# Optimization experiments

Measured on AMD Instinct MI355X. Metric: run time of the kernel, lower is better.

## Reference

```python
import jax, jax.numpy as jnp
import numpy as np

VOCAB = 256
HDC_DIM = 4096
DECAY = 0.95
B, T = 8, 2048


def setup_inputs() -> dict:
    key = jax.random.key(0)
    k_cb, k_idx = jax.random.split(key)
    # bipolar codebook: sign of gaussian, zeros mapped to +1 (prob-0 event but faithful)
    cb = jnp.sign(jax.random.normal(k_cb, (VOCAB, HDC_DIM), dtype=jnp.float32))
    cb = jnp.where(cb == 0, 1.0, cb)
    idx = jax.random.randint(k_idx, (B, T), 0, VOCAB)
    return {"char_codebook": cb, "idx": idx}


def _encode_trigrams(char_codebook, idx):
    chars = char_codebook[idx]                       # (B, T, D)
    chars_m1 = jnp.roll(chars, 1, axis=1).at[:, 0, :].set(0.0)
    chars_m2 = jnp.roll(chars, 2, axis=1).at[:, :2, :].set(0.0)
    trigrams = chars * jnp.roll(chars_m1, 1, axis=-1) * jnp.roll(chars_m2, 2, axis=-1)
    return 0.7 * trigrams + 0.3 * chars


def _decay_matrix(T, dtype):
    i = jnp.arange(T)
    diffs = (i[:, None] - i[None, :]).astype(dtype)  # (T, T)
    m = jnp.where(diffs >= 0, jnp.asarray(DECAY, dtype) ** diffs, 0.0)
    return m / jnp.sum(m, axis=-1, keepdims=True)    # row-normalized causal decay


def reference(char_codebook, idx):
    hdc = _encode_trigrams(char_codebook, idx)       # (B, T, D)
    M = _decay_matrix(hdc.shape[1], hdc.dtype)       # (T, T)
    # context[t] = sum_i M[t, i] * hdc[i]  -> one dense matmul as in the original
    return jnp.einsum("ts,bsd->btd", M, hdc)
```

## Files before the change

kernel.cpp:

```cpp
#include <hip/hip_runtime.h>


#define VOCAB   256
#define D_      4096
#define T_      2048
#define B_      8
#define DEC     0.95f
#define CHUNK   128
#define WARM    192
#define NCH     (T_/CHUNK)
#define THREADS 128
#define DGRP    (D_/(THREADS*8))
#define ROWB    (D_/8)

__device__ unsigned char g_P1[VOCAB*ROWB];
__device__ unsigned char g_P2[VOCAB*ROWB];
__device__ unsigned char g_P3[VOCAB*ROWB];

__global__ __launch_bounds__(256) void pack_kernel(const float* __restrict__ cb) {
    int gid = blockIdx.x * 256 + threadIdx.x;
    int r   = gid >> 9;
    int byt = gid & 511;
    const float* row = cb + r * D_;
    unsigned b1 = 0, b2 = 0, b3 = 0;
#pragma unroll
    for (int j = 0; j < 8; ++j) {
        int d = byt * 8 + j;
        unsigned s1 = __float_as_uint(row[d]) >> 31;
        unsigned s2 = __float_as_uint(row[(d - 1) & (D_ - 1)]) >> 31;
        unsigned s3 = __float_as_uint(row[(d - 2) & (D_ - 1)]) >> 31;
        b1 |= s1 << j; b2 |= s2 << j; b3 |= s3 << j;
    }
    g_P1[gid] = (unsigned char)b1;
    g_P2[gid] = (unsigned char)b2;
    g_P3[gid] = (unsigned char)b3;
}

__global__ __launch_bounds__(THREADS) void hdc_kernel(const int* __restrict__ idx,
                                                      float* __restrict__ out) {
    const int b  = blockIdx.z;
    const int ch = blockIdx.y;
    const int dg = blockIdx.x;
    const int t0 = ch * CHUNK;
    const int ts = (t0 - WARM > 0) ? (t0 - WARM) : 0;
    const int t1 = t0 + CHUNK;
    const int lo = (ts - 2 > 0) ? (ts - 2) : 0;

    __shared__ int sidx[CHUNK + WARM + 2];
    for (int t = lo + threadIdx.x; t < t1; t += THREADS)
        sidx[t - lo] = idx[b * T_ + t];
    __syncthreads();

    const int i = dg * THREADS + threadIdx.x;

    float acc[8];
#pragma unroll
    for (int j = 0; j < 8; ++j) acc[j] = 0.0f;

    const int wsteps = t0 - ts;
#pragma unroll 4
    for (int k = 0; k < wsteps; ++k) {
        int t = ts + k;
        int r1 = sidx[t - lo];
        unsigned ub1 = g_P1[r1 * ROWB + i];
        unsigned n8 = 0;
        float magp = 1.0f, magn = -0.4f;
        if (t >= 2) {
            int r2 = sidx[t - 1 - lo], r3 = sidx[t - 2 - lo];
            n8 = (unsigned)(g_P2[r2 * ROWB + i] ^ g_P3[r3 * ROWB + i]);
        } else {
            magp = 0.3f; magn = 0.3f;
        }
#pragma unroll
        for (int j = 0; j < 8; ++j) {
            float mag    = ((n8 >> j) & 1u) ? magn : magp;
            unsigned sgn = (ub1 << (31 - j)) & 0x80000000u;
            float v      = __uint_as_float(__float_as_uint(mag) ^ sgn);
            acc[j] = fmaf(acc[j], DEC, v);
        }
    }

    float qn = powf(DEC, (float)(t0 + 1));
    float* ob = out + (size_t)(b * T_) * D_ + (size_t)i * 8;
#pragma unroll 2
    for (int k = 0; k < CHUNK; ++k) {
        int t = t0 + k;
        int r1 = sidx[t - lo];
        unsigned ub1 = g_P1[r1 * ROWB + i];
        unsigned n8 = 0;
        float magp = 1.0f, magn = -0.4f;
        if (t >= 2) {
            int r2 = sidx[t - 1 - lo], r3 = sidx[t - 2 - lo];
            n8 = (unsigned)(g_P2[r2 * ROWB + i] ^ g_P3[r3 * ROWB + i]);
        } else {
            magp = 0.3f; magn = 0.3f;
        }
        float invn = (1.0f - DEC) / (1.0f - qn);
        float res[8];
#pragma unroll
        for (int j = 0; j < 8; ++j) {
            float mag    = ((n8 >> j) & 1u) ? magn : magp;
            unsigned sgn = (ub1 << (31 - j)) & 0x80000000u;
            float v      = __uint_as_float(__float_as_uint(mag) ^ sgn);
            acc[j] = fmaf(acc[j], DEC, v);
            res[j] = acc[j] * invn;
        }
        float4* o = (float4*)(ob + (size_t)t * D_);
        o[0] = make_float4(res[0], res[1], res[2], res[3]);
        o[1] = make_float4(res[4], res[5], res[6], res[7]);
        qn *= DEC;
    }
}

extern "C" void kernel_launch(void* const* d_in, const int* in_sizes, int n_in,
                              void* d_out, int out_size, void* d_ws, size_t ws_size,
                              hipStream_t stream) {
    const float* cb  = (const float*)d_in[0];
    const int*   idx = (const int*)d_in[1];
    float*       out = (float*)d_out;

    pack_kernel<<<dim3((VOCAB * ROWB) / 256), dim3(256), 0, stream>>>(cb);
    hdc_kernel<<<dim3(DGRP, NCH, B_), dim3(THREADS), 0, stream>>>(idx, out);
}
```

Baseline: 349.7 us.

## Replace warm-up recomputation with exact chunked scan via carry propagation

Drops the approximate 192-step warm-up per chunk and uses an exact three-phase chunked scan instead: per-chunk local states, a serial carry pass across chunks, then an emit pass seeded with the carry. Chunk size shrinks to 32, which raises the block count, and the normalisation factors are precomputed into a table. This removes redundant recurrence work but adds two extra kernel launches and global round trips for the state and carry buffers. The carry kernel runs serially over 64 chunks per element.

Result: faster. 304.3 us (-13.0%).

```diff
diff --git a/kernel.cpp b/kernel.cpp
--- a/kernel.cpp
+++ b/kernel.cpp
@@ -6,8 +6,7 @@
 #define T_      2048
 #define B_      8
 #define DEC     0.95f
-#define CHUNK   128
-#define WARM    192
+#define CHUNK   32
 #define NCH     (T_/CHUNK)
 #define THREADS 128
 #define DGRP    (D_/(THREADS*8))
@@ -16,6 +15,9 @@
 __device__ unsigned char g_P1[VOCAB*ROWB];
 __device__ unsigned char g_P2[VOCAB*ROWB];
 __device__ unsigned char g_P3[VOCAB*ROWB];
+__device__ float g_invn[T_];
+__device__ float g_S[B_*NCH*D_];
+__device__ float g_C[B_*NCH*D_];
 
 __global__ __launch_bounds__(256) void pack_kernel(const float* __restrict__ cb) {
     int gid = blockIdx.x * 256 + threadIdx.x;
@@ -34,81 +36,110 @@
     g_P1[gid] = (unsigned char)b1;
     g_P2[gid] = (unsigned char)b2;
     g_P3[gid] = (unsigned char)b3;
+    if (gid < T_)
+        g_invn[gid] = (1.0f - DEC) / (1.0f - powf(DEC, (float)(gid + 1)));
 }
 
-__global__ __launch_bounds__(THREADS) void hdc_kernel(const int* __restrict__ idx,
-                                                      float* __restrict__ out) {
+__device__ __forceinline__ void bind_step(unsigned ub1, unsigned n8,
+                                          float magp, float magn, float* acc) {
+#pragma unroll
+    for (int j = 0; j < 8; ++j) {
+        float mag    = ((n8 >> j) & 1u) ? magn : magp;
+        unsigned sgn = (ub1 << (31 - j)) & 0x80000000u;
+        float v      = __uint_as_float(__float_as_uint(mag) ^ sgn);
+        acc[j] = fmaf(acc[j], DEC, v);
+    }
+}
+
+__global__ __launch_bounds__(THREADS) void states_kernel(const int* __restrict__ idx) {
     const int b  = blockIdx.z;
     const int ch = blockIdx.y;
     const int dg = blockIdx.x;
     const int t0 = ch * CHUNK;
-    const int ts = (t0 - WARM > 0) ? (t0 - WARM) : 0;
-    const int t1 = t0 + CHUNK;
-    const int lo = (ts - 2 > 0) ? (ts - 2) : 0;
+    const int lo = (t0 - 2 > 0) ? (t0 - 2) : 0;
 
-    __shared__ int sidx[CHUNK + WARM + 2];
-    for (int t = lo + threadIdx.x; t < t1; t += THREADS)
-        sidx[t - lo] = idx[b * T_ + t];
+    __shared__ int sidx[CHUNK + 2];
+    if (threadIdx.x < (unsigned)(t0 + CHUNK - lo))
+        sidx[threadIdx.x] = idx[b * T_ + lo + threadIdx.x];
+    __syncthreads();
+
+    const int i = dg * THREADS + threadIdx.x;
+    float acc[8];
+#pragma unroll
+    for (int j = 0; j < 8; ++j) acc[j] = 0.0f;
+
+#pragma unroll 4
+    for (int k = 0; k < CHUNK; ++k) {
+        int t = t0 + k;
+        int r1 = sidx[t - lo];
+        unsigned ub1 = g_P1[r1 * ROWB + i];
+        unsigned n8 = 0; float magp = 1.0f, magn = -0.4f;
+        if (t >= 2) {
+            int r2 = sidx[t - 1 - lo], r3 = sidx[t - 2 - lo];
+            n8 = (unsigned)(g_P2[r2 * ROWB + i] ^ g_P3[r3 * ROWB + i]);
+        } else { magp = 0.3f; magn = 0.3f; }
+        bind_step(ub1, n8, magp, magn, acc);
+    }
+
+    float* S = g_S + (size_t)(b * NCH + ch) * D_ + (size_t)i * 8;
+    ((float4*)S)[0] = make_float4(acc[0], acc[1], acc[2], acc[3]);
+    ((float4*)S)[1] = make_float4(acc[4], acc[5], acc[6], acc[7]);
+}
+
+__global__ __launch_bounds__(256) void carry_kernel() {
+    int g = blockIdx.x * 256 + threadIdx.x;
+    int b = g >> 12;
+    int d = g & (D_ - 1);
+    float dch = powf(DEC, (float)CHUNK);
+    float c = 0.0f;
+#pragma unroll 8
+    for (int ch = 0; ch < NCH; ++ch) {
+        size_t o = (size_t)(b * NCH + ch) * D_ + d;
+        g_C[o] = c;
+        c = fmaf(c, dch, g_S[o]);
+    }
+}
+
+__global__ __launch_bounds__(THREADS) void emit_kernel(const int* __restrict__ idx,
+                                                       float* __restrict__ out) {
+    const int b  = blockIdx.z;
+    const int ch = blockIdx.y;
+    const int dg = blockIdx.x;
+    const int t0 = ch * CHUNK;
+    const int lo = (t0 - 2 > 0) ? (t0 - 2) : 0;
+
+    __shared__ int   sidx[CHUNK + 2];
+    __shared__ float sinv[CHUNK];
+    if (threadIdx.x < (unsigned)(t0 + CHUNK - lo))
+        sidx[threadIdx.x] = idx[b * T_ + lo + threadIdx.x];
+    if (threadIdx.x < CHUNK)
+        sinv[threadIdx.x] = g_invn[t0 + threadIdx.x];
     __syncthreads();
 
     const int i = dg * THREADS + threadIdx.x;
 
-    float acc[8];
-#pragma unroll
-    for (int j = 0; j < 8; ++j) acc[j] = 0.0f;
+    const float* C = g_C + (size_t)(b * NCH + ch) * D_ + (size_t)i * 8;
+    float4 c0 = ((const float4*)C)[0];
+    float4 c1 = ((const float4*)C)[1];
+    float acc[8] = {c0.x, c0.y, c0.z, c0.w, c1.x, c1.y, c1.z, c1.w};
 
-    const int wsteps = t0 - ts;
+    float* ob = out + (size_t)(b * T_) * D_ + (size_t)i * 8;
 #pragma unroll 4
-    for (int k = 0; k < wsteps; ++k) {
-        int t = ts + k;
-        int r1 = sidx[t - lo];
-        unsigned ub1 = g_P1[r1 * ROWB + i];
-        unsigned n8 = 0;
-        float magp = 1.0f, magn = -0.4f;
-        if (t >= 2) {
-            int r2 = sidx[t - 1 - lo], r3 = sidx[t - 2 - lo];
-            n8 = (unsigned)(g_P2[r2 * ROWB + i] ^ g_P3[r3 * ROWB + i]);
-        } else {
-            magp = 0.3f; magn = 0.3f;
-        }
-#pragma unroll
-        for (int j = 0; j < 8; ++j) {
-            float mag    = ((n8 >> j) & 1u) ? magn : magp;
-            unsigned sgn = (ub1 << (31 - j)) & 0x80000000u;
-            float v      = __uint_as_float(__float_as_uint(mag) ^ sgn);
-            acc[j] = fmaf(acc[j], DEC, v);
-        }
-    }
-
-    float qn = powf(DEC, (float)(t0 + 1));
-    float* ob = out + (size_t)(b * T_) * D_ + (size_t)i * 8;
-#pragma unroll 2
     for (int k = 0; k < CHUNK; ++k) {
         int t = t0 + k;
         int r1 = sidx[t - lo];
         unsigned ub1 = g_P1[r1 * ROWB + i];
-        unsigned n8 = 0;
-        float magp = 1.0f, magn = -0.4f;
+        unsigned n8 = 0; float magp = 1.0f, magn = -0.4f;
         if (t >= 2) {
             int r2 = sidx[t - 1 - lo], r3 = sidx[t - 2 - lo];
             n8 = (unsigned)(g_P2[r2 * ROWB + i] ^ g_P3[r3 * ROWB + i]);
-        } else {
-            magp = 0.3f; magn = 0.3f;
-        }
-        float invn = (1.0f - DEC) / (1.0f - qn);
-        float res[8];
-#pragma unroll
-        for (int j = 0; j < 8; ++j) {
-            float mag    = ((n8 >> j) & 1u) ? magn : magp;
-            unsigned sgn = (ub1 << (31 - j)) & 0x80000000u;
-            float v      = __uint_as_float(__float_as_uint(mag) ^ sgn);
-            acc[j] = fmaf(acc[j], DEC, v);
-            res[j] = acc[j] * invn;
-        }
+        } else { magp = 0.3f; magn = 0.3f; }
+        bind_step(ub1, n8, magp, magn, acc);
+
+        float invn = sinv[k];
         float4* o = (float4*)(ob + (size_t)t * D_);
-        o[0] = make_float4(res[0], res[1], res[2], res[3]);
-        o[1] = make_float4(res[4], res[5], res[6], res[7]);
-        qn *= DEC;
+        o[0] = make_float4(acc[0]*invn, acc[1]*invn, acc[2]*invn, acc[3]*invn);
+        o[1] = make_float4(acc[4]*invn, acc[5]*invn, acc[6]*invn, acc[7]*invn);
     }
 }
 
@@ -119,6 +150,8 @@
     const int*   idx = (const int*)d_in[1];
     float*       out = (float*)d_out;
 
-    pack_kernel<<<dim3((VOCAB * ROWB) / 256), dim3(256), 0, stream>>>(cb);
-    hdc_kernel<<<dim3(DGRP, NCH, B_), dim3(THREADS), 0, stream>>>(idx, out);
+    pack_kernel  <<<dim3((VOCAB * ROWB) / 256), dim3(256), 0, stream>>>(cb);
+    states_kernel<<<dim3(DGRP, NCH, B_), dim3(THREADS), 0, stream>>>(idx);
+    carry_kernel <<<dim3((B_ * D_) / 256), dim3(256), 0, stream>>>();
+    emit_kernel  <<<dim3(DGRP, NCH, B_), dim3(THREADS), 0, stream>>>(idx, out);
 }
```
